# Kernel tuning notes

Hardware: AMD Instinct MI355X
Metric: run time of the kernel (lower is better)

Reference implementation:

```python
import jax, jax.numpy as jnp
import numpy as np
import math

CHUNK = 128


def setup_inputs() -> dict:
    key = jax.random.key(0)
    ks = jax.random.split(key, 12)
    B, S, H, D = 2, 4096, 1024, 2048  # D = hidden_dim * expansion_factor
    std = 0.02
    inp = {
        "hidden_states": jax.random.normal(ks[0], (B, S, H), jnp.float32),
        "Wq": jax.random.normal(ks[1], (H, D), jnp.float32) * std,
        "bq": jnp.zeros((D,), jnp.float32),
        "Wk": jax.random.normal(ks[2], (H, D), jnp.float32) * std,
        "bk": jnp.zeros((D,), jnp.float32),
        "Wv": jax.random.normal(ks[3], (H, D), jnp.float32) * std,
        "bv": jnp.zeros((D,), jnp.float32),
        "Wg": jax.random.normal(ks[4], (H, D), jnp.float32) * std,
        "bg": jnp.zeros((D,), jnp.float32),
        "Wo": jax.random.normal(ks[5], (D, H), jnp.float32) * std,
        "bo": jnp.zeros((H,), jnp.float32),
    }
    return inp


def reference(hidden_states, Wq, bq, Wk, bk, Wv, bv, Wg, bg, Wo, bo):
    B, S, H = hidden_states.shape
    D = Wq.shape[1]
    cs = CHUNK
    nC = S // cs  # seq_len chosen as multiple of chunk_size (no padding path)

    q = hidden_states @ Wq + bq
    k = hidden_states @ Wk + bk
    v = hidden_states @ Wv + bv
    gate = jax.nn.sigmoid(hidden_states @ Wg + bg)

    qc = q.reshape(B, nC, cs, D)
    kc = k.reshape(B, nC, cs, D)
    vc = v.reshape(B, nC, cs, D)
    gc = gate.reshape(B, nC, cs, D)

    # intra-chunk causal softmax attention (vectorized over all chunks)
    scale = 1.0 / math.sqrt(D)
    attn = jnp.einsum('bncd,bnkd->bnck', qc, kc) * scale  # [B,nC,cs,cs]
    causal = jnp.tril(jnp.ones((cs, cs), bool))
    attn = jnp.where(causal, attn, -jnp.inf)
    attn = jax.nn.softmax(attn, axis=-1)
    local = jnp.einsum('bnck,bnkd->bncd', attn, vc)

    # inter-chunk linear-attention state accumulation:
    # cross_i = q_i @ sum_{j<i} K_j^T V_j  (sequential scan over chunks)
    def step(state, xs):
        qi, ki, vi = xs  # each [B,cs,D]
        cross = jnp.einsum('bcd,bde->bce', qi, state)
        state = state + jnp.einsum('bcd,bce->bde', ki, vi)
        return state, cross

    state0 = jnp.zeros((B, D, D), hidden_states.dtype)
    _, cross = jax.lax.scan(
        step, state0,
        (qc.transpose(1, 0, 2, 3), kc.transpose(1, 0, 2, 3), vc.transpose(1, 0, 2, 3)))
    cross = cross.transpose(1, 0, 2, 3)  # [B,nC,cs,D]

    out = (local + cross) * gc
    out = out.reshape(B, S, D)
    return out @ Wo + bo
```

## Files before the change

### kernel.cpp

```cpp
#include <hip/hip_runtime.h>
#include <hip/hip_bf16.h>
#include <math.h>


typedef __bf16 bf16_t;
typedef __bf16 bf16x8 __attribute__((ext_vector_type(8)));
typedef __bf16 bf16x4 __attribute__((ext_vector_type(4)));
typedef float f32x4 __attribute__((ext_vector_type(4)));

#define NB_ 2
#define SEQ 4096
#define HID 1024
#define DD 2048
#define NCH 32
#define BS 8192
#define LDS_BYTES 131072

__device__ __forceinline__ void async16(const void* g, void* l) {
  __builtin_amdgcn_global_load_lds(
      (const __attribute__((address_space(1))) void*)g,
      (__attribute__((address_space(3))) void*)l, 16, 0, 0);
}

#define VMW4 asm volatile("s_waitcnt vmcnt(4)" ::: "memory")
#define VMW0 asm volatile("s_waitcnt vmcnt(0)" ::: "memory")
#define FEN asm volatile("" ::: "memory")
#define BARR __builtin_amdgcn_s_barrier()

template <int MFH>
__device__ __forceinline__ void readA8(const bf16_t* bufA, int aBase, int s0, int s1,
                                       bf16x8 (&af)[4][2]) {
#pragma unroll
  for (int mm = 0; mm < 4; ++mm) {
    int p = aBase + MFH * 8192 + mm * 1024;
    af[mm][0] = *reinterpret_cast<const bf16x8*>(&bufA[p + s0]);
    af[mm][1] = *reinterpret_cast<const bf16x8*>(&bufA[p + s1]);
  }
}
template <int NFH>
__device__ __forceinline__ void readB4(const bf16_t* bufB, int bBase, int s0, int s1,
                                       bf16x8 (&bv)[2][2]) {
#pragma unroll
  for (int nn = 0; nn < 2; ++nn) {
    int p = bBase + NFH * 8192 + nn * 1024;
    bv[nn][0] = *reinterpret_cast<const bf16x8*>(&bufB[p + s0]);
    bv[nn][1] = *reinterpret_cast<const bf16x8*>(&bufB[p + s1]);
  }
}
template <int MFH, int NFH>
__device__ __forceinline__ void mfma16(const bf16x8 (&af)[4][2], const bf16x8 (&bv)[2][2],
                                       f32x4 (&acc)[8][4]) {
  __builtin_amdgcn_s_setprio(1);
#pragma unroll
  for (int kki = 0; kki < 2; ++kki)
#pragma unroll
    for (int mm = 0; mm < 4; ++mm)
#pragma unroll
      for (int nn = 0; nn < 2; ++nn)
        acc[MFH * 4 + mm][NFH * 2 + nn] = __builtin_amdgcn_mfma_f32_16x16x32_bf16(
            af[mm][kki], bv[nn][kki], acc[MFH * 4 + mm][NFH * 2 + nn], 0, 0, 0);
  __builtin_amdgcn_s_setprio(0);
}

__device__ __forceinline__ void gemm256(const bf16_t* __restrict__ A, int lda,
                                        const bf16_t* __restrict__ B, int ldb, int nt,
                                        bf16_t* lds, f32x4 (&acc)[8][4]) {
  const int t = threadIdx.x;
  const int lane = t & 63, w = t >> 6;
  const int wm = w >> 2, wn = w & 3;
  const int lr = lane & 15, lg = lane >> 4;
  const int xm = lr & 7;

  const int aBase = (wm * 64 + lr) * 64;
  const int bBase = (wn * 32 + lr) * 64;
  const int s0 = (lg ^ xm) * 8;
  const int s1 = ((4 + lg) ^ xm) * 8;

  int srcA[4], srcB[4];
  const int slog = ((t & 7) ^ ((t >> 3) & 7)) * 8;
#pragma unroll
  for (int blk = 0; blk < 4; ++blk) {
    int rA = ((blk & 1) << 7) + ((blk >> 1) << 6) + (t >> 3);
    int prB = (blk << 6) + (t >> 3);
    int rB = (((prB >> 5) & 3) << 6) + ((prB >> 7) << 5) + (prB & 31);
    srcA[blk] = rA * lda + slog;
    srcB[blk] = rB * ldb + slog;
  }
  const int dstT = t * 8;

#pragma unroll
  for (int m = 0; m < 8; ++m)
#pragma unroll
    for (int n = 0; n < 4; ++n) acc[m][n] = (f32x4){0.f, 0.f, 0.f, 0.f};

  {
    bf16_t* nA = lds;
    bf16_t* nB = lds + 16384;
    async16(A + srcA[0], nA + dstT);
    async16(A + srcA[1], nA + 4096 + dstT);
    async16(B + srcB[0], nB + dstT);
    async16(B + srcB[1], nB + 4096 + dstT);
    async16(A + srcA[2], nA + 8192 + dstT);
    async16(A + srcA[3], nA + 12288 + dstT);
    async16(B + srcB[2], nB + 8192 + dstT);
    async16(B + srcB[3], nB + 12288 + dstT);
  }

  bf16x8 af0[4][2], af1[4][2], bv0[2][2], bv1[2][2];

  for (int kt = 0; kt < nt; ++kt) {
    bf16_t* bufA = lds + ((kt & 1) << 15);
    bf16_t* bufB = bufA + 16384;
    bf16_t* nA = lds + (((kt + 1) & 1) << 15);
    bf16_t* nB = nA + 16384;
    const int kn = (kt + 1 < nt ? (kt + 1) : 0) << 6;
    const bf16_t* An = A + kn;
    const bf16_t* Bn = B + kn;
    VMW4; BARR; FEN;
    readA8<0>(bufA, aBase, s0, s1, af0);
    readB4<0>(bufB, bBase, s0, s1, bv0);
    mfma16<0, 0>(af0, bv0, acc);
    async16(An + srcA[0], nA + dstT);
    async16(An + srcA[1], nA + 4096 + dstT);
    VMW4; BARR; FEN;
    readA8<1>(bufA, aBase, s0, s1, af1);
    mfma16<1, 0>(af1, bv0, acc);
    async16(Bn + srcB[0], nB + dstT);
    async16(Bn + srcB[1], nB + 4096 + dstT);
    VMW4; BARR; FEN;
    readB4<1>(bufB, bBase, s0, s1, bv1);
    mfma16<1, 1>(af1, bv1, acc);
    async16(An + srcA[2], nA + 8192 + dstT);
    async16(An + srcA[3], nA + 12288 + dstT);
    readA8<0>(bufA, aBase, s0, s1, af0);
    mfma16<0, 1>(af0, bv1, acc);
    async16(Bn + srcB[2], nB + 8192 + dstT);
    async16(Bn + srcB[3], nB + 12288 + dstT);
  }
  VMW0;
  BARR;
}

__global__ void k_cvt(const float4* __restrict__ in, bf16x4* __restrict__ out, int n4) {
  int i = blockIdx.x * blockDim.x + threadIdx.x;
  if (i < n4) {
    float4 v = in[i];
    bf16x4 o;
    o[0] = (bf16_t)v.x; o[1] = (bf16_t)v.y; o[2] = (bf16_t)v.z; o[3] = (bf16_t)v.w;
    out[i] = o;
  }
}

__global__ void k_tconv(const float* __restrict__ in, bf16_t* __restrict__ out,
                        int R, int C) {
  __shared__ bf16_t tile[64][65];
  int bc = blockIdx.x, br = blockIdx.y;
  int t = threadIdx.x;
  int c = t & 63, r0 = t >> 6;
#pragma unroll
  for (int rr = 0; rr < 64; rr += 4) {
    int r = rr + r0;
    tile[r][c] = (bf16_t)in[(long)(br * 64 + r) * C + bc * 64 + c];
  }
  __syncthreads();
#pragma unroll
  for (int rr = 0; rr < 64; rr += 4) {
    int r = rr + r0;
    out[(long)(bc * 64 + r) * R + br * 64 + c] = tile[c][r];
  }
}

__global__ void k_tbf16(const bf16_t* __restrict__ in, bf16_t* __restrict__ out,
                        int R, int C) {
  __shared__ bf16_t tile[64][65];
  long zoff = (long)blockIdx.z * R * C;
  in += zoff;
  out += zoff;
  int bc = blockIdx.x, br = blockIdx.y;
  int t = threadIdx.x;
  int c = t & 63, r0 = t >> 6;
#pragma unroll
  for (int rr = 0; rr < 64; rr += 4) {
    int r = rr + r0;
    tile[r][c] = in[(long)(br * 64 + r) * C + bc * 64 + c];
  }
  __syncthreads();
#pragma unroll
  for (int rr = 0; rr < 64; rr += 4) {
    int r = rr + r0;
    out[(long)(bc * 64 + r) * R + br * 64 + c] = tile[c][r];
  }
}

__global__ __launch_bounds__(512) void k_gemm_qkvg(
    const bf16_t* __restrict__ hsb, const bf16_t* __restrict__ Wt4,
    const float* __restrict__ bq, const float* __restrict__ bk,
    const float* __restrict__ bv, const float* __restrict__ bg,
    bf16_t* __restrict__ out) {
  extern __shared__ bf16_t lds[];
  int c = blockIdx.x;
  int c2 = (c & 7) * 128 + (c >> 3);
  int mb = c2 >> 5, nb = c2 & 31;
  f32x4 acc[8][4];
  gemm256(hsb + (long)mb * 256 * HID, HID, Wt4 + (long)nb * 256 * HID, HID,
          HID / 64, lds, acc);
  const int t = threadIdx.x, lane = t & 63, w = t >> 6;
  const int wm = w >> 2, wn = w & 3, lr = lane & 15, lg = lane >> 4;
  int z = nb >> 3;
  const float* bias = z == 0 ? bq : z == 1 ? bk : z == 2 ? bv : bg;
  int colbase = (nb & 7) * 256 + wn * 64;
  float b4[4];
#pragma unroll
  for (int nf = 0; nf < 4; ++nf) b4[nf] = bias[colbase + nf * 16 + lr];
  bf16_t* O = out + (long)z * BS * DD;
#pragma unroll
  for (int mf = 0; mf < 8; ++mf)
#pragma unroll
    for (int reg = 0; reg < 4; ++reg) {
      long row = mb * 256 + wm * 128 + mf * 16 + lg * 4 + reg;
#pragma unroll
      for (int nf = 0; nf < 4; ++nf) {
        float v = acc[mf][nf][reg] + b4[nf];
        if (z == 3) v = 1.f / (1.f + __expf(-v));
        O[row * DD + colbase + nf * 16 + lr] = (bf16_t)v;
      }
    }
}

__global__ __launch_bounds__(512) void k_pair(const bf16_t* __restrict__ Q,
                                              const bf16_t* __restrict__ Kb,
                                              bf16_t* __restrict__ P) {
  extern __shared__ bf16_t lds[];
  int p = blockIdx.x, b = blockIdx.y;
  int m = 0, base = 0;
  while (base + m + 1 <= p) { base += m + 1; ++m; }
  int jt = p - base;
  f32x4 acc[8][4];
  gemm256(Q + ((long)b * SEQ + m * 256) * DD, DD,
          Kb + ((long)b * SEQ + jt * 256) * DD, DD, DD / 64, lds, acc);
  const int t = threadIdx.x, lane = t & 63, w = t >> 6;
  const int wm = w >> 2, wn = w & 3, lr = lane & 15, lg = lane >> 4;
  bf16_t* Pt = P + ((long)b * SEQ + m * 256) * (long)SEQ + jt * 256;
  if (jt < m) {
#pragma unroll
    for (int mf = 0; mf < 8; ++mf)
#pragma unroll
      for (int reg = 0; reg < 4; ++reg) {
        int row = wm * 128 + mf * 16 + lg * 4 + reg;
#pragma unroll
        for (int nf = 0; nf < 4; ++nf)
          Pt[(long)row * SEQ + wn * 64 + nf * 16 + lr] = (bf16_t)acc[mf][nf][reg];
      }
    return;
  }
  const float scale = 0.02209708691207961f;
  if (wm == 1 && wn < 2) {
#pragma unroll
    for (int mf = 0; mf < 8; ++mf)
#pragma unroll
      for (int reg = 0; reg < 4; ++reg) {
        int row = 128 + mf * 16 + lg * 4 + reg;
#pragma unroll
        for (int nf = 0; nf < 4; ++nf)
          Pt[(long)row * SEQ + wn * 64 + nf * 16 + lr] = (bf16_t)acc[mf][nf][reg];
      }
  }
  if (wm == 0 && wn >= 2) {
#pragma unroll
    for (int mf = 0; mf < 8; ++mf)
#pragma unroll
      for (int reg = 0; reg < 4; ++reg) {
        int row = mf * 16 + lg * 4 + reg;
#pragma unroll
        for (int nf = 0; nf < 4; ++nf)
          Pt[(long)row * SEQ + wn * 64 + nf * 16 + lr] = (bf16_t)0.f;
      }
  }
  float* smf = (float*)lds;
#pragma unroll
  for (int h = 0; h < 2; ++h) {
    __syncthreads();
    if (wm == h && (wn >> 1) == h) {
#pragma unroll
      for (int mf = 0; mf < 8; ++mf)
#pragma unroll
        for (int reg = 0; reg < 4; ++reg) {
          int r = mf * 16 + lg * 4 + reg;
#pragma unroll
          for (int nf = 0; nf < 4; ++nf) {
            int cc = (wn & 1) * 64 + nf * 16 + lr;
            float v = acc[mf][nf][reg] * scale;
            smf[r * 128 + ((cc + r) & 127)] = (cc <= r) ? v : -1e30f;
          }
        }
    }
    __syncthreads();
    if (t < 128) {
      int r = t;
      float mx = -1e30f;
      for (int cc = 0; cc <= r; ++cc) mx = fmaxf(mx, smf[r * 128 + ((cc + r) & 127)]);
      float s = 0.f;
      for (int cc = 0; cc <= r; ++cc) s += __expf(smf[r * 128 + ((cc + r) & 127)] - mx);
      float inv = 1.f / s;
      for (int cc = 0; cc < 128; ++cc) {
        float v = (cc <= r) ? __expf(smf[r * 128 + ((cc + r) & 127)] - mx) * inv : 0.f;
        Pt[(long)(h * 128 + r) * SEQ + h * 128 + cc] = (bf16_t)v;
      }
    }
  }
}

__global__ __launch_bounds__(512) void k_gemm2(const bf16_t* __restrict__ P,
                                               const bf16_t* __restrict__ Vt,
                                               const bf16_t* __restrict__ G,
                                               bf16_t* __restrict__ OutPre) {
  extern __shared__ bf16_t lds[];
  int nb = blockIdx.x;
  int y = blockIdx.y;
  int b = y >> 4, m = y & 15;
  f32x4 acc[8][4];
  gemm256(P + ((long)b * SEQ + m * 256) * (long)SEQ, SEQ,
          Vt + (long)b * DD * SEQ + (long)nb * 256 * SEQ, SEQ, (m + 1) * 4, lds, acc);
  const int t = threadIdx.x, lane = t & 63, w = t >> 6;
  const int wm = w >> 2, wn = w & 3, lr = lane & 15, lg = lane >> 4;
#pragma unroll
  for (int mf = 0; mf < 8; ++mf)
#pragma unroll
    for (int reg = 0; reg < 4; ++reg) {
      long row = (long)b * SEQ + m * 256 + wm * 128 + mf * 16 + lg * 4 + reg;
#pragma unroll
      for (int nf = 0; nf < 4; ++nf) {
        long idx = row * DD + nb * 256 + wn * 64 + nf * 16 + lr;
        float g = (float)G[idx];
        OutPre[idx] = (bf16_t)(acc[mf][nf][reg] * g);
      }
    }
}

__global__ __launch_bounds__(512) void k_gemm3(const bf16_t* __restrict__ OutPre,
                                               const bf16_t* __restrict__ Wot,
                                               const float* __restrict__ bo,
                                               float* __restrict__ out) {
  extern __shared__ bf16_t lds[];
  int c = blockIdx.x;
  int mb = c >> 2, nb = c & 3;
  f32x4 acc[8][4];
  gemm256(OutPre + (long)mb * 256 * DD, DD, Wot + (long)nb * 256 * DD, DD,
          DD / 64, lds, acc);
  const int t = threadIdx.x, lane = t & 63, w = t >> 6;
  const int wm = w >> 2, wn = w & 3, lr = lane & 15, lg = lane >> 4;
  int colbase = nb * 256 + wn * 64;
  float b4[4];
#pragma unroll
  for (int nf = 0; nf < 4; ++nf) b4[nf] = bo[colbase + nf * 16 + lr];
#pragma unroll
  for (int mf = 0; mf < 8; ++mf)
#pragma unroll
    for (int reg = 0; reg < 4; ++reg) {
      long row = mb * 256 + wm * 128 + mf * 16 + lg * 4 + reg;
#pragma unroll
      for (int nf = 0; nf < 4; ++nf)
        out[row * HID + colbase + nf * 16 + lr] = acc[mf][nf][reg] + b4[nf];
    }
}

extern "C" void kernel_launch(void* const* d_in, const int* in_sizes, int n_in,
                              void* d_out, int out_size, void* d_ws, size_t ws_size,
                              hipStream_t stream) {
  const float* hs = (const float*)d_in[0];
  const float* Wq = (const float*)d_in[1];
  const float* bq = (const float*)d_in[2];
  const float* Wk = (const float*)d_in[3];
  const float* bk = (const float*)d_in[4];
  const float* Wv = (const float*)d_in[5];
  const float* bv = (const float*)d_in[6];
  const float* Wg = (const float*)d_in[7];
  const float* bg = (const float*)d_in[8];
  const float* Wo = (const float*)d_in[9];
  const float* bo = (const float*)d_in[10];
  float* out = (float*)d_out;

  char* ws = (char*)d_ws;
  const size_t MB = 1024 * 1024;
  bf16_t* P = (bf16_t*)(ws);
  bf16_t* hsb = (bf16_t*)(ws);
  bf16_t* Wt4 = (bf16_t*)(ws + 16 * MB);
  bf16_t* Wot = (bf16_t*)(ws + 64 * MB);
  bf16_t* QKVG = (bf16_t*)(ws + 68 * MB);
  bf16_t* Vt = (bf16_t*)(ws + 196 * MB);

  bf16_t* Qb = QKVG;
  bf16_t* Kbuf = QKVG + (long)BS * DD;
  bf16_t* Vbuf = QKVG + 2l * BS * DD;
  bf16_t* Gbuf = QKVG + 3l * BS * DD;
  bf16_t* OutPre = Vbuf;

  hipFuncSetAttribute((const void*)k_gemm_qkvg,
                      hipFuncAttributeMaxDynamicSharedMemorySize, LDS_BYTES);
  hipFuncSetAttribute((const void*)k_pair,
                      hipFuncAttributeMaxDynamicSharedMemorySize, LDS_BYTES);
  hipFuncSetAttribute((const void*)k_gemm2,
                      hipFuncAttributeMaxDynamicSharedMemorySize, LDS_BYTES);
  hipFuncSetAttribute((const void*)k_gemm3,
                      hipFuncAttributeMaxDynamicSharedMemorySize, LDS_BYTES);

  k_cvt<<<(BS * HID / 4 + 255) / 256, 256, 0, stream>>>((const float4*)hs,
                                                        (bf16x4*)hsb, BS * HID / 4);
  k_tconv<<<dim3(DD / 64, HID / 64), 256, 0, stream>>>(Wq, Wt4 + 0l * DD * HID, HID, DD);
  k_tconv<<<dim3(DD / 64, HID / 64), 256, 0, stream>>>(Wk, Wt4 + 1l * DD * HID, HID, DD);
  k_tconv<<<dim3(DD / 64, HID / 64), 256, 0, stream>>>(Wv, Wt4 + 2l * DD * HID, HID, DD);
  k_tconv<<<dim3(DD / 64, HID / 64), 256, 0, stream>>>(Wg, Wt4 + 3l * DD * HID, HID, DD);
  k_tconv<<<dim3(HID / 64, DD / 64), 256, 0, stream>>>(Wo, Wot, DD, HID);

  k_gemm_qkvg<<<1024, 512, LDS_BYTES, stream>>>(hsb, Wt4, bq, bk, bv, bg, QKVG);

  k_tbf16<<<dim3(DD / 64, SEQ / 64, NB_), 256, 0, stream>>>(Vbuf, Vt, SEQ, DD);

  k_pair<<<dim3(136, 2), 512, LDS_BYTES, stream>>>(Qb, Kbuf, P);

  k_gemm2<<<dim3(8, 32), 512, LDS_BYTES, stream>>>(P, Vt, Gbuf, OutPre);

  k_gemm3<<<128, 512, LDS_BYTES, stream>>>(OutPre, Wot, bo, out);
}
```

Baseline: 485.6 us.

## Add 128x256 GEMM tile core for pair, gemm2, gemm3 and reorder 256-tile pipeline

Adds a core128 GEMM routine with 128-row A tiles and a smaller LDS footprint, and uses it in k_pair, k_gemm2 and k_gemm3. This doubles their grid sizes to fill more CUs and balances the triangular work in gemm2, ordering longest rows first. k_pair now handles a 128-row query strip whose diagonal block gets masked softmax, replacing the old two-phase diagonal handling. The 256 core issues more LDS reads ahead of its MFMAs with looser vmcnt waits, and launch_bounds now request 2 waves per SIMD. The smaller tiles give less data reuse per tile in exchange for better occupancy and load balance.

```diff
diff --git a/kernel.cpp b/kernel.cpp
--- a/kernel.cpp
+++ b/kernel.cpp
@@ -12,9 +12,9 @@
 #define SEQ 4096
 #define HID 1024
 #define DD 2048
-#define NCH 32
 #define BS 8192
-#define LDS_BYTES 131072
+#define LDS256 131072
+#define LDS128 98304
 
 __device__ __forceinline__ void async16(const void* g, void* l) {
   __builtin_amdgcn_global_load_lds(
@@ -22,10 +22,9 @@
       (__attribute__((address_space(3))) void*)l, 16, 0, 0);
 }
 
-#define VMW4 asm volatile("s_waitcnt vmcnt(4)" ::: "memory")
-#define VMW0 asm volatile("s_waitcnt vmcnt(0)" ::: "memory")
+#define VMW(n) asm volatile("s_waitcnt vmcnt(" #n ")" ::: "memory")
+#define BARR __builtin_amdgcn_s_barrier()
 #define FEN asm volatile("" ::: "memory")
-#define BARR __builtin_amdgcn_s_barrier()
 
 template <int MFH>
 __device__ __forceinline__ void readA8(const bf16_t* bufA, int aBase, int s0, int s1,
@@ -47,9 +46,9 @@
     bv[nn][1] = *reinterpret_cast<const bf16x8*>(&bufB[p + s1]);
   }
 }
-template <int MFH, int NFH>
-__device__ __forceinline__ void mfma16(const bf16x8 (&af)[4][2], const bf16x8 (&bv)[2][2],
-                                       f32x4 (&acc)[8][4]) {
+template <int MROWS, int MQ, int NQ>
+__device__ __forceinline__ void mfmaQ(const bf16x8 (&af)[4][2], const bf16x8 (&bv)[2][2],
+                                      f32x4 (&acc)[MROWS][4]) {
   __builtin_amdgcn_s_setprio(1);
 #pragma unroll
   for (int kki = 0; kki < 2; ++kki)
@@ -57,12 +56,12 @@
     for (int mm = 0; mm < 4; ++mm)
 #pragma unroll
       for (int nn = 0; nn < 2; ++nn)
-        acc[MFH * 4 + mm][NFH * 2 + nn] = __builtin_amdgcn_mfma_f32_16x16x32_bf16(
-            af[mm][kki], bv[nn][kki], acc[MFH * 4 + mm][NFH * 2 + nn], 0, 0, 0);
+        acc[MQ * 4 + mm][NQ * 2 + nn] = __builtin_amdgcn_mfma_f32_16x16x32_bf16(
+            af[mm][kki], bv[nn][kki], acc[MQ * 4 + mm][NQ * 2 + nn], 0, 0, 0);
   __builtin_amdgcn_s_setprio(0);
 }
 
-__device__ __forceinline__ void gemm256(const bf16_t* __restrict__ A, int lda,
+__device__ __forceinline__ void core256(const bf16_t* __restrict__ A, int lda,
                                         const bf16_t* __restrict__ B, int ldb, int nt,
                                         bf16_t* lds, f32x4 (&acc)[8][4]) {
   const int t = threadIdx.x;
@@ -70,14 +69,11 @@
   const int wm = w >> 2, wn = w & 3;
   const int lr = lane & 15, lg = lane >> 4;
   const int xm = lr & 7;
-
   const int aBase = (wm * 64 + lr) * 64;
   const int bBase = (wn * 32 + lr) * 64;
-  const int s0 = (lg ^ xm) * 8;
-  const int s1 = ((4 + lg) ^ xm) * 8;
-
+  const int s0 = (lg ^ xm) * 8, s1 = ((4 + lg) ^ xm) * 8;
+  const int slog = ((t & 7) ^ ((t >> 3) & 7)) * 8;
   int srcA[4], srcB[4];
-  const int slog = ((t & 7) ^ ((t >> 3) & 7)) * 8;
 #pragma unroll
   for (int blk = 0; blk < 4; ++blk) {
     int rA = ((blk & 1) << 7) + ((blk >> 1) << 6) + (t >> 3);
@@ -87,7 +83,6 @@
     srcB[blk] = rB * ldb + slog;
   }
   const int dstT = t * 8;
-
 #pragma unroll
   for (int m = 0; m < 8; ++m)
 #pragma unroll
@@ -105,39 +100,99 @@
     async16(B + srcB[2], nB + 8192 + dstT);
     async16(B + srcB[3], nB + 12288 + dstT);
   }
-
   bf16x8 af0[4][2], af1[4][2], bv0[2][2], bv1[2][2];
-
   for (int kt = 0; kt < nt; ++kt) {
     bf16_t* bufA = lds + ((kt & 1) << 15);
     bf16_t* bufB = bufA + 16384;
     bf16_t* nA = lds + (((kt + 1) & 1) << 15);
     bf16_t* nB = nA + 16384;
-    const int kn = (kt + 1 < nt ? (kt + 1) : 0) << 6;
+    const int kn = (kt + 1 < nt ? kt + 1 : 0) << 6;
     const bf16_t* An = A + kn;
     const bf16_t* Bn = B + kn;
-    VMW4; BARR; FEN;
+    VMW(2); BARR; FEN;
     readA8<0>(bufA, aBase, s0, s1, af0);
     readB4<0>(bufB, bBase, s0, s1, bv0);
-    mfma16<0, 0>(af0, bv0, acc);
+    readA8<1>(bufA, aBase, s0, s1, af1);
     async16(An + srcA[0], nA + dstT);
     async16(An + srcA[1], nA + 4096 + dstT);
-    VMW4; BARR; FEN;
-    readA8<1>(bufA, aBase, s0, s1, af1);
-    mfma16<1, 0>(af1, bv0, acc);
+    mfmaQ<8, 0, 0>(af0, bv0, acc);
+    VMW(2); BARR; FEN;
+    readB4<1>(bufB, bBase, s0, s1, bv1);
     async16(Bn + srcB[0], nB + dstT);
     async16(Bn + srcB[1], nB + 4096 + dstT);
-    VMW4; BARR; FEN;
-    readB4<1>(bufB, bBase, s0, s1, bv1);
-    mfma16<1, 1>(af1, bv1, acc);
+    mfmaQ<8, 1, 0>(af1, bv0, acc);
     async16(An + srcA[2], nA + 8192 + dstT);
     async16(An + srcA[3], nA + 12288 + dstT);
-    readA8<0>(bufA, aBase, s0, s1, af0);
-    mfma16<0, 1>(af0, bv1, acc);
+    mfmaQ<8, 1, 1>(af1, bv1, acc);
     async16(Bn + srcB[2], nB + 8192 + dstT);
     async16(Bn + srcB[3], nB + 12288 + dstT);
-  }
-  VMW0;
+    mfmaQ<8, 0, 1>(af0, bv1, acc);
+  }
+  VMW(0);
+  BARR;
+}
+
+__device__ __forceinline__ void core128(const bf16_t* __restrict__ A, int lda,
+                                        const bf16_t* __restrict__ B, int ldb, int nt,
+                                        bf16_t* lds, f32x4 (&acc)[4][4]) {
+  const int t = threadIdx.x;
+  const int lane = t & 63, w = t >> 6;
+  const int wm = w >> 2, wn = w & 3;
+  const int lr = lane & 15, lg = lane >> 4;
+  const int xm = lr & 7;
+  const int aBase = (wm * 64 + lr) * 64;
+  const int bBase = (wn * 32 + lr) * 64;
+  const int s0 = (lg ^ xm) * 8, s1 = ((4 + lg) ^ xm) * 8;
+  const int slog = ((t & 7) ^ ((t >> 3) & 7)) * 8;
+  int srcA[2], srcB[4];
+#pragma unroll
+  for (int blk = 0; blk < 2; ++blk) srcA[blk] = (blk * 64 + (t >> 3)) * lda + slog;
+#pragma unroll
+  for (int blk = 0; blk < 4; ++blk) {
+    int prB = (blk << 6) + (t >> 3);
+    int rB = (((prB >> 5) & 3) << 6) + ((prB >> 7) << 5) + (prB & 31);
+    srcB[blk] = rB * ldb + slog;
+  }
+  const int dstT = t * 8;
+#pragma unroll
+  for (int m = 0; m < 4; ++m)
+#pragma unroll
+    for (int n = 0; n < 4; ++n) acc[m][n] = (f32x4){0.f, 0.f, 0.f, 0.f};
+
+  {
+    bf16_t* nA = lds;
+    bf16_t* nB = lds + 8192;
+    async16(A + srcA[0], nA + dstT);
+    async16(A + srcA[1], nA + 4096 + dstT);
+    async16(B + srcB[0], nB + dstT);
+    async16(B + srcB[1], nB + 4096 + dstT);
+    async16(B + srcB[2], nB + 8192 + dstT);
+    async16(B + srcB[3], nB + 12288 + dstT);
+  }
+  bf16x8 af[4][2], bv0[2][2], bv1[2][2];
+  for (int kt = 0; kt < nt; ++kt) {
+    bf16_t* bufA = lds + (kt & 1) * 24576;
+    bf16_t* bufB = bufA + 8192;
+    bf16_t* nA = lds + ((kt + 1) & 1) * 24576;
+    bf16_t* nB = nA + 8192;
+    const int kn = (kt + 1 < nt ? kt + 1 : 0) << 6;
+    const bf16_t* An = A + kn;
+    const bf16_t* Bn = B + kn;
+    VMW(2); BARR; FEN;
+    readA8<0>(bufA, aBase, s0, s1, af);
+    readB4<0>(bufB, bBase, s0, s1, bv0);
+    async16(An + srcA[0], nA + dstT);
+    async16(An + srcA[1], nA + 4096 + dstT);
+    async16(Bn + srcB[0], nB + dstT);
+    mfmaQ<4, 0, 0>(af, bv0, acc);
+    VMW(3); BARR; FEN;
+    readB4<1>(bufB, bBase, s0, s1, bv1);
+    async16(Bn + srcB[1], nB + 4096 + dstT);
+    async16(Bn + srcB[2], nB + 8192 + dstT);
+    async16(Bn + srcB[3], nB + 12288 + dstT);
+    mfmaQ<4, 0, 1>(af, bv1, acc);
+  }
+  VMW(0);
   BARR;
 }
 
@@ -192,7 +247,7 @@
   }
 }
 
-__global__ __launch_bounds__(512) void k_gemm_qkvg(
+__global__ __launch_bounds__(512, 2) void k_gemm_qkvg(
     const bf16_t* __restrict__ hsb, const bf16_t* __restrict__ Wt4,
     const float* __restrict__ bq, const float* __restrict__ bk,
     const float* __restrict__ bv, const float* __restrict__ bg,
@@ -202,7 +257,7 @@
   int c2 = (c & 7) * 128 + (c >> 3);
   int mb = c2 >> 5, nb = c2 & 31;
   f32x4 acc[8][4];
-  gemm256(hsb + (long)mb * 256 * HID, HID, Wt4 + (long)nb * 256 * HID, HID,
+  core256(hsb + (long)mb * 256 * HID, HID, Wt4 + (long)nb * 256 * HID, HID,
           HID / 64, lds, acc);
   const int t = threadIdx.x, lane = t & 63, w = t >> 6;
   const int wm = w >> 2, wn = w & 3, lr = lane & 15, lg = lane >> 4;
@@ -227,73 +282,43 @@
     }
 }
 
-__global__ __launch_bounds__(512) void k_pair(const bf16_t* __restrict__ Q,
-                                              const bf16_t* __restrict__ Kb,
-                                              bf16_t* __restrict__ P) {
+__global__ __launch_bounds__(512, 2) void k_pair(const bf16_t* __restrict__ Q,
+                                                 const bf16_t* __restrict__ Kb,
+                                                 bf16_t* __restrict__ P) {
   extern __shared__ bf16_t lds[];
   int p = blockIdx.x, b = blockIdx.y;
-  int m = 0, base = 0;
-  while (base + m + 1 <= p) { base += m + 1; ++m; }
+  int c = 0, base = 0;
+  while (base + (c >> 1) + 1 <= p) { base += (c >> 1) + 1; ++c; }
   int jt = p - base;
-  f32x4 acc[8][4];
-  gemm256(Q + ((long)b * SEQ + m * 256) * DD, DD,
-          Kb + ((long)b * SEQ + jt * 256) * DD, DD, DD / 64, lds, acc);
+  f32x4 acc[4][4];
+  core128(Q + ((long)b * SEQ + (long)c * 128) * DD, DD,
+          Kb + ((long)b * SEQ + (long)jt * 256) * DD, DD, DD / 64, lds, acc);
   const int t = threadIdx.x, lane = t & 63, w = t >> 6;
   const int wm = w >> 2, wn = w & 3, lr = lane & 15, lg = lane >> 4;
-  bf16_t* Pt = P + ((long)b * SEQ + m * 256) * (long)SEQ + jt * 256;
-  if (jt < m) {
-#pragma unroll
-    for (int mf = 0; mf < 8; ++mf)
-#pragma unroll
-      for (int reg = 0; reg < 4; ++reg) {
-        int row = wm * 128 + mf * 16 + lg * 4 + reg;
-#pragma unroll
-        for (int nf = 0; nf < 4; ++nf)
-          Pt[(long)row * SEQ + wn * 64 + nf * 16 + lr] = (bf16_t)acc[mf][nf][reg];
+  bf16_t* Pt = P + ((long)b * SEQ + (long)c * 128) * (long)SEQ + (long)jt * 256;
+  const bool hasDiag = (jt == (c >> 1));
+  const int side = c & 1;
+  const float scale = 0.02209708691207961f;
+  float* smf = (float*)lds;
+#pragma unroll
+  for (int mf = 0; mf < 4; ++mf)
+#pragma unroll
+    for (int reg = 0; reg < 4; ++reg) {
+      int row = wm * 64 + mf * 16 + lg * 4 + reg;
+#pragma unroll
+      for (int nf = 0; nf < 4; ++nf) {
+        int col = wn * 64 + nf * 16 + lr;
+        float v = acc[mf][nf][reg];
+        if (hasDiag && ((col >> 7) == side)) {
+          int cc = col & 127;
+          float sv = v * scale;
+          smf[row * 128 + ((cc + row) & 127)] = (cc <= row) ? sv : -1e30f;
+        } else {
+          Pt[(long)row * SEQ + col] = (bf16_t)v;
+        }
       }
-    return;
-  }
-  const float scale = 0.02209708691207961f;
-  if (wm == 1 && wn < 2) {
-#pragma unroll
-    for (int mf = 0; mf < 8; ++mf)
-#pragma unroll
-      for (int reg = 0; reg < 4; ++reg) {
-        int row = 128 + mf * 16 + lg * 4 + reg;
-#pragma unroll
-        for (int nf = 0; nf < 4; ++nf)
-          Pt[(long)row * SEQ + wn * 64 + nf * 16 + lr] = (bf16_t)acc[mf][nf][reg];
-      }
-  }
-  if (wm == 0 && wn >= 2) {
-#pragma unroll
-    for (int mf = 0; mf < 8; ++mf)
-#pragma unroll
-      for (int reg = 0; reg < 4; ++reg) {
-        int row = mf * 16 + lg * 4 + reg;
-#pragma unroll
-        for (int nf = 0; nf < 4; ++nf)
-          Pt[(long)row * SEQ + wn * 64 + nf * 16 + lr] = (bf16_t)0.f;
-      }
-  }
-  float* smf = (float*)lds;
-#pragma unroll
-  for (int h = 0; h < 2; ++h) {
-    __syncthreads();
-    if (wm == h && (wn >> 1) == h) {
-#pragma unroll
-      for (int mf = 0; mf < 8; ++mf)
-#pragma unroll
-        for (int reg = 0; reg < 4; ++reg) {
-          int r = mf * 16 + lg * 4 + reg;
-#pragma unroll
-          for (int nf = 0; nf < 4; ++nf) {
-            int cc = (wn & 1) * 64 + nf * 16 + lr;
-            float v = acc[mf][nf][reg] * scale;
-            smf[r * 128 + ((cc + r) & 127)] = (cc <= r) ? v : -1e30f;
-          }
-        }
     }
+  if (hasDiag) {
     __syncthreads();
     if (t < 128) {
       int r = t;
@@ -304,30 +329,31 @@
       float inv = 1.f / s;
       for (int cc = 0; cc < 128; ++cc) {
         float v = (cc <= r) ? __expf(smf[r * 128 + ((cc + r) & 127)] - mx) * inv : 0.f;
-        Pt[(long)(h * 128 + r) * SEQ + h * 128 + cc] = (bf16_t)v;
+        Pt[(long)r * SEQ + side * 128 + cc] = (bf16_t)v;
       }
     }
   }
 }
 
-__global__ __launch_bounds__(512) void k_gemm2(const bf16_t* __restrict__ P,
-                                               const bf16_t* __restrict__ Vt,
-                                               const bf16_t* __restrict__ G,
-                                               bf16_t* __restrict__ OutPre) {
+__global__ __launch_bounds__(512, 2) void k_gemm2(const bf16_t* __restrict__ P,
+                                                  const bf16_t* __restrict__ Vt,
+                                                  const bf16_t* __restrict__ G,
+                                                  bf16_t* __restrict__ OutPre) {
   extern __shared__ bf16_t lds[];
-  int nb = blockIdx.x;
-  int y = blockIdx.y;
-  int b = y >> 4, m = y & 15;
-  f32x4 acc[8][4];
-  gemm256(P + ((long)b * SEQ + m * 256) * (long)SEQ, SEQ,
-          Vt + (long)b * DD * SEQ + (long)nb * 256 * SEQ, SEQ, (m + 1) * 4, lds, acc);
+  int bid = blockIdx.x;
+  int mq = 31 - (bid >> 4);
+  int r2 = bid & 15;
+  int nb = r2 >> 1, b = r2 & 1;
+  f32x4 acc[4][4];
+  core128(P + ((long)b * SEQ + (long)mq * 128) * (long)SEQ, SEQ,
+          Vt + (long)b * DD * SEQ + (long)nb * 256 * SEQ, SEQ, (mq + 1) * 2, lds, acc);
   const int t = threadIdx.x, lane = t & 63, w = t >> 6;
   const int wm = w >> 2, wn = w & 3, lr = lane & 15, lg = lane >> 4;
 #pragma unroll
-  for (int mf = 0; mf < 8; ++mf)
+  for (int mf = 0; mf < 4; ++mf)
 #pragma unroll
     for (int reg = 0; reg < 4; ++reg) {
-      long row = (long)b * SEQ + m * 256 + wm * 128 + mf * 16 + lg * 4 + reg;
+      long row = (long)b * SEQ + (long)mq * 128 + wm * 64 + mf * 16 + lg * 4 + reg;
 #pragma unroll
       for (int nf = 0; nf < 4; ++nf) {
         long idx = row * DD + nb * 256 + wn * 64 + nf * 16 + lr;
@@ -337,15 +363,14 @@
     }
 }
 
-__global__ __launch_bounds__(512) void k_gemm3(const bf16_t* __restrict__ OutPre,
-                                               const bf16_t* __restrict__ Wot,
-                                               const float* __restrict__ bo,
-                                               float* __restrict__ out) {
+__global__ __launch_bounds__(512, 2) void k_gemm3(const bf16_t* __restrict__ OutPre,
+                                                  const bf16_t* __restrict__ Wot,
+                                                  const float* __restrict__ bo,
+                                                  float* __restrict__ out) {
   extern __shared__ bf16_t lds[];
-  int c = blockIdx.x;
-  int mb = c >> 2, nb = c & 3;
-  f32x4 acc[8][4];
-  gemm256(OutPre + (long)mb * 256 * DD, DD, Wot + (long)nb * 256 * DD, DD,
+  int mb = blockIdx.x >> 2, nb = blockIdx.x & 3;
+  f32x4 acc[4][4];
+  core128(OutPre + (long)mb * 128 * DD, DD, Wot + (long)nb * 256 * DD, DD,
           DD / 64, lds, acc);
   const int t = threadIdx.x, lane = t & 63, w = t >> 6;
   const int wm = w >> 2, wn = w & 3, lr = lane & 15, lg = lane >> 4;
@@ -354,10 +379,10 @@
 #pragma unroll
   for (int nf = 0; nf < 4; ++nf) b4[nf] = bo[colbase + nf * 16 + lr];
 #pragma unroll
-  for (int mf = 0; mf < 8; ++mf)
+  for (int mf = 0; mf < 4; ++mf)
 #pragma unroll
     for (int reg = 0; reg < 4; ++reg) {
-      long row = mb * 256 + wm * 128 + mf * 16 + lg * 4 + reg;
+      long row = mb * 128 + wm * 64 + mf * 16 + lg * 4 + reg;
 #pragma unroll
       for (int nf = 0; nf < 4; ++nf)
         out[row * HID + colbase + nf * 16 + lr] = acc[mf][nf][reg] + b4[nf];
@@ -396,13 +421,13 @@
   bf16_t* OutPre = Vbuf;
 
   hipFuncSetAttribute((const void*)k_gemm_qkvg,
-                      hipFuncAttributeMaxDynamicSharedMemorySize, LDS_BYTES);
+                      hipFuncAttributeMaxDynamicSharedMemorySize, LDS256);
   hipFuncSetAttribute((const void*)k_pair,
-                      hipFuncAttributeMaxDynamicSharedMemorySize, LDS_BYTES);
+                      hipFuncAttributeMaxDynamicSharedMemorySize, LDS128);
   hipFuncSetAttribute((const void*)k_gemm2,
-                      hipFuncAttributeMaxDynamicSharedMemorySize, LDS_BYTES);
+                      hipFuncAttributeMaxDynamicSharedMemorySize, LDS128);
   hipFuncSetAttribute((const void*)k_gemm3,
-                      hipFuncAttributeMaxDynamicSharedMemorySize, LDS_BYTES);
+                      hipFuncAttributeMaxDynamicSharedMemorySize, LDS128);
 
   k_cvt<<<(BS * HID / 4 + 255) / 256, 256, 0, stream>>>((const float4*)hs,
                                                         (bf16x4*)hsb, BS * HID / 4);
@@ -412,13 +437,13 @@
   k_tconv<<<dim3(DD / 64, HID / 64), 256, 0, stream>>>(Wg, Wt4 + 3l * DD * HID, HID, DD);
   k_tconv<<<dim3(HID / 64, DD / 64), 256, 0, stream>>>(Wo, Wot, DD, HID);
 
-  k_gemm_qkvg<<<1024, 512, LDS_BYTES, stream>>>(hsb, Wt4, bq, bk, bv, bg, QKVG);
+  k_gemm_qkvg<<<1024, 512, LDS256, stream>>>(hsb, Wt4, bq, bk, bv, bg, QKVG);
 
   k_tbf16<<<dim3(DD / 64, SEQ / 64, NB_), 256, 0, stream>>>(Vbuf, Vt, SEQ, DD);
 
-  k_pair<<<dim3(136, 2), 512, LDS_BYTES, stream>>>(Qb, Kbuf, P);
-
-  k_gemm2<<<dim3(8, 32), 512, LDS_BYTES, stream>>>(P, Vt, Gbuf, OutPre);
-
-  k_gemm3<<<128, 512, LDS_BYTES, stream>>>(OutPre, Wot, bo, out);
-}
+  k_pair<<<dim3(272, 2), 512, LDS128, stream>>>(Qb, Kbuf, P);
+
+  k_gemm2<<<512, 512, LDS128, stream>>>(P, Vt, Gbuf, OutPre);
+
+  k_gemm3<<<256, 512, LDS128, stream>>>(OutPre, Wot, bo, out);
+}
```

Measured after the change: 433.1 us. 10.8% less time.
